# Performance work log

Measured on AMD Instinct MI355X. Metric: run time of the kernel, lower is better.

## Reference

```python
import jax, jax.numpy as jnp
import numpy as np
import math

EMBED = 1024
FF = 4096
HEADS = 16
HEAD = EMBED // HEADS
EPS = 1e-5


def new_gelu(x):
    c = math.sqrt(2.0 / math.pi)
    return 0.5 * x * (1.0 + jnp.tanh(c * (x + 0.044715 * x ** 3)))


def layer_norm(x, g, b):
    mu = jnp.mean(x, axis=-1, keepdims=True)
    var = jnp.var(x, axis=-1, keepdims=True)
    return (x - mu) * jax.lax.rsqrt(var + EPS) * g + b


def setup_inputs() -> dict:
    key = jax.random.key(0)
    ks = jax.random.split(key, 16)
    s = 0.02
    d = {
        'x': jax.random.normal(ks[0], (2, 2048, EMBED), jnp.float32),
        'Wq': jax.random.normal(ks[1], (EMBED, EMBED)) * s,
        'bq': jnp.zeros((EMBED,)),
        'Wk': jax.random.normal(ks[2], (EMBED, EMBED)) * s,
        'bk': jnp.zeros((EMBED,)),
        'Wv': jax.random.normal(ks[3], (EMBED, EMBED)) * s,
        'bv': jnp.zeros((EMBED,)),
        'Wp': jax.random.normal(ks[4], (EMBED, EMBED)) * s,
        'bp': jnp.zeros((EMBED,)),
        'W1': jax.random.normal(ks[5], (EMBED, FF)) * s,
        'b1': jnp.zeros((FF,)),
        'W2': jax.random.normal(ks[6], (FF, EMBED)) * s,
        'b2': jnp.zeros((EMBED,)),
        'g1': jnp.ones((EMBED,)), 'be1': jnp.zeros((EMBED,)),
        'g2': jnp.ones((EMBED,)), 'be2': jnp.zeros((EMBED,)),
    }
    return d


def reference(x, Wq, bq, Wk, bk, Wv, bv, Wp, bp, W1, b1, W2, b2, g1, be1, g2, be2):
    B, S, D = x.shape
    h = layer_norm(x, g1, be1)
    # project and split heads: [B,S,D] -> [B,H,S,Hd]
    def heads(y):
        return y.reshape(B, S, HEADS, HEAD).transpose(0, 2, 1, 3)
    Q = heads(h @ Wq + bq)
    K = heads(h @ Wk + bk)
    V = heads(h @ Wv + bv)
    att = jnp.einsum('bhqd,bhkd->bhqk', Q, K) / math.sqrt(HEAD)
    att = jax.nn.softmax(att, axis=-1)
    out = jnp.einsum('bhqk,bhkd->bhqd', att, V)
    out = out.transpose(0, 2, 1, 3).reshape(B, S, D)
    x = x + (out @ Wp + bp)  # dropout p=0 / eval -> identity
    h2 = layer_norm(x, g2, be2)
    x = x + (new_gelu(h2 @ W1 + b1) @ W2 + b2)
    return x
```

## Files before the change

### kernel.cpp

```cpp
#include <hip/hip_runtime.h>
#include <cstdint>


typedef __attribute__((ext_vector_type(8))) short short8;
typedef __attribute__((ext_vector_type(4))) float f32x4;

#define QSCL 0.18033688011112042f

__device__ __forceinline__ float bf2f(unsigned short u) {
    union { unsigned int i; float f; } v; v.i = ((unsigned int)u) << 16; return v.f;
}
__device__ __forceinline__ unsigned short f2bf(float f) {
    union { float f; unsigned int i; } v; v.f = f;
    unsigned int u = v.i;
    u += 0x7fff + ((u >> 16) & 1);
    return (unsigned short)(u >> 16);
}
__device__ __forceinline__ float gelu_f(float x) {
    float u = 0.7978845608028654f * (x + 0.044715f * x * x * x);
    float t = 1.f - 2.f / (__expf(2.f * u) + 1.f);
    return 0.5f * x * (1.f + t);
}
__device__ __forceinline__ void async16(const unsigned short* gp, unsigned short* lp) {
    __builtin_amdgcn_global_load_lds(
        (__attribute__((address_space(1))) void*)(gp),
        (__attribute__((address_space(3))) void*)(lp),
        16, 0, 0);
}

__device__ __forceinline__ void ln_dev(
    const float* __restrict__ x, const float* __restrict__ g,
    const float* __restrict__ b, unsigned short* __restrict__ o,
    int row, float* red)
{
    const int tid = threadIdx.x;
    const float4 v = ((const float4*)(x + (size_t)row * 1024))[tid];
    float f0 = v.x, f1 = v.y, f2 = v.z, f3 = v.w;
    float sum = f0 + f1 + f2 + f3;
    float sq  = f0 * f0 + f1 * f1 + f2 * f2 + f3 * f3;
    for (int off = 1; off < 64; off <<= 1) {
        sum += __shfl_xor(sum, off);
        sq  += __shfl_xor(sq,  off);
    }
    int wv = tid >> 6, ln = tid & 63;
    if (ln == 0) { red[wv] = sum; red[4 + wv] = sq; }
    __syncthreads();
    sum = red[0] + red[1] + red[2] + red[3];
    sq  = red[4] + red[5] + red[6] + red[7];
    float mu  = sum * (1.0f / 1024.0f);
    float var = sq  * (1.0f / 1024.0f) - mu * mu;
    float rsd = rsqrtf(fmaxf(var, 0.f) + 1e-5f);
    const float4 gg = ((const float4*)g)[tid];
    const float4 bb = ((const float4*)b)[tid];
    unsigned short* orow = o + (size_t)row * 1024;
    orow[4 * tid + 0] = f2bf((f0 - mu) * rsd * gg.x + bb.x);
    orow[4 * tid + 1] = f2bf((f1 - mu) * rsd * gg.y + bb.y);
    orow[4 * tid + 2] = f2bf((f2 - mu) * rsd * gg.z + bb.z);
    orow[4 * tid + 3] = f2bf((f3 - mu) * rsd * gg.w + bb.w);
}

__device__ __forceinline__ void transpose_dev(
    const float* __restrict__ in, unsigned short* __restrict__ out,
    int R, int C, int inStride, int bx, int by, unsigned short* tile ,
    float scale)
{
    const int tx = threadIdx.x & 15, ty = threadIdx.x >> 4;
    const int c0 = bx * 64, r0 = by * 64;
#pragma unroll
    for (int i = 0; i < 4; ++i) {
        int r = ty + 16 * i;
        float4 v = *(const float4*)(in + (size_t)(r0 + r) * inStride + c0 + tx * 4);
        tile[r * 70 + tx * 4 + 0] = f2bf(v.x * scale);
        tile[r * 70 + tx * 4 + 1] = f2bf(v.y * scale);
        tile[r * 70 + tx * 4 + 2] = f2bf(v.z * scale);
        tile[r * 70 + tx * 4 + 3] = f2bf(v.w * scale);
    }
    __syncthreads();
#pragma unroll
    for (int i = 0; i < 4; ++i) {
        int c = ty * 4 + i;
        ushort4 o;
        o.x = tile[(tx * 4 + 0) * 70 + c];
        o.y = tile[(tx * 4 + 1) * 70 + c];
        o.z = tile[(tx * 4 + 2) * 70 + c];
        o.w = tile[(tx * 4 + 3) * 70 + c];
        *(ushort4*)(out + (size_t)(c0 + c) * R + r0 + tx * 4) = o;
    }
}

__global__ __launch_bounds__(256) void ln_k(
    const float* __restrict__ x, const float* __restrict__ g,
    const float* __restrict__ b, unsigned short* __restrict__ o)
{
    __shared__ float red[8];
    ln_dev(x, g, b, o, blockIdx.x, red);
}
__global__ __launch_bounds__(256) void transpose_f2b(
    const float* __restrict__ in, unsigned short* __restrict__ out,
    int R, int C, int inStride, float scale)
{
    __shared__ unsigned short tile[64 * 70];
    transpose_dev(in, out, R, C, inStride, blockIdx.x, blockIdx.y, tile, scale);
}

__global__ __launch_bounds__(256) void prep1_k(
    const float* __restrict__ x,
    const float* __restrict__ g1, const float* __restrict__ be1,
    const float* __restrict__ Wq, const float* __restrict__ Wk,
    const float* __restrict__ Wv,
    const float* __restrict__ bq, const float* __restrict__ bk,
    const float* __restrict__ bv,
    unsigned short* __restrict__ hb,
    unsigned short* __restrict__ WTqkv,
    float* __restrict__ bcat)
{
    __shared__ unsigned short smem[64 * 70];
    const int b = blockIdx.x;
    if (b < 4096) {
        ln_dev(x, g1, be1, hb, b, (float*)smem);
    } else if (b < 4096 + 768) {
        int t = b - 4096;
        int w = t >> 8;
        int tt = t & 255;
        const float* W = (w == 0) ? Wq : (w == 1) ? Wk : Wv;
        transpose_dev(W, WTqkv + (size_t)w * 1024 * 1024,
                      1024, 1024, 1024, tt & 15, tt >> 4, smem,
                      (w == 0) ? QSCL : 1.f);
    } else {
        int i = (b - 4096 - 768) * 256 + threadIdx.x;
        float v = (i < 1024) ? bq[i] * QSCL : (i < 2048) ? bk[i - 1024] : bv[i - 2048];
        bcat[i] = v;
    }
}

__global__ __launch_bounds__(256) void prep2_k(
    const float* __restrict__ x1,
    const float* __restrict__ g2, const float* __restrict__ be2,
    const float* __restrict__ W1, const float* __restrict__ W2,
    unsigned short* __restrict__ h2,
    unsigned short* __restrict__ WT1,
    unsigned short* __restrict__ WT2)
{
    __shared__ unsigned short smem[64 * 70];
    const int b = blockIdx.x;
    if (b < 4096) {
        ln_dev(x1, g2, be2, h2, b, (float*)smem);
    } else if (b < 4096 + 1024) {
        int t = b - 4096;
        transpose_dev(W1, WT1, 1024, 4096, 4096, t & 63, t >> 6, smem, 1.f);
    } else {
        int t = b - 4096 - 1024;
        transpose_dev(W2, WT2, 4096, 1024, 1024, t & 15, t >> 4, smem, 1.f);
    }
}

__global__ __launch_bounds__(256) void vt_k(
    const unsigned short* __restrict__ src, int stride,
    unsigned short* __restrict__ Vt)
{
    __shared__ unsigned short tile[64][70];
    const int tx = threadIdx.x & 15, ty = threadIdx.x >> 4;
    const int t0 = blockIdx.x * 64;
    const int bh = blockIdx.y;
    const int bo = (bh >> 4) * 2048;
    const int ho = (bh & 15) * 64;
    const unsigned short* s = src + (size_t)bo * stride + ho;
#pragma unroll
    for (int i = 0; i < 4; ++i) {
        int r = ty + 16 * i;
        ushort4 v = *(const ushort4*)(s + (size_t)(t0 + r) * stride + tx * 4);
        tile[r][tx * 4 + 0] = v.x;
        tile[r][tx * 4 + 1] = v.y;
        tile[r][tx * 4 + 2] = v.z;
        tile[r][tx * 4 + 3] = v.w;
    }
    __syncthreads();
    unsigned short* dst = Vt + (size_t)bh * 64 * 2048;
    const int hh = tx >> 3;
    const int uu = (tx & 7) * 2;
#pragma unroll
    for (int i = 0; i < 4; ++i) {
        int d = ty * 4 + i;
        ushort4 o;
        o.x = tile[32 * hh + uu][d];
        o.y = tile[32 * hh + 16 + uu][d];
        o.z = tile[32 * hh + uu + 1][d];
        o.w = tile[32 * hh + 17 + uu][d];
        *(ushort4*)(dst + (size_t)d * 2048 + t0 + tx * 4) = o;
    }
}

__global__ __launch_bounds__(256, 3) void gemm_bt(
    const unsigned short* __restrict__ A,
    const unsigned short* __restrict__ Bt,
    const float* __restrict__ bias,
    const float* __restrict__ res,
    void* __restrict__ C,
    int M, int N, int K, int ldb, int dogelu, int out32, float bscale)
{
    __shared__ unsigned short sA[2 * 128 * 32];
    __shared__ unsigned short sB[2 * 128 * 32];
    const int tid  = threadIdx.x;
    const int wave = tid >> 6;
    const int lane = tid & 63;
    const int quad = lane >> 4;
    const int l15  = lane & 15;
    const int bm = blockIdx.y * 128;
    const int bn = blockIdx.x * 128;
    const int wM = (wave >> 1) * 64;
    const int wN = (wave & 1) * 64;

    f32x4 acc[4][4];
#pragma unroll
    for (int i = 0; i < 4; ++i)
#pragma unroll
        for (int j = 0; j < 4; ++j)
            acc[i][j] = (f32x4){0.f, 0.f, 0.f, 0.f};

    const int rowS = tid >> 2;
    const int kcS  = (tid & 3) * 8;
    const unsigned short* gA  = A  + (size_t)(bm + rowS) * K + kcS;
    const unsigned short* gA2 = gA + (size_t)64 * K;
    const unsigned short* gB  = Bt + (size_t)(bn + rowS) * ldb + kcS;
    const unsigned short* gB2 = gB + (size_t)64 * ldb;
    unsigned short* lA  = sA + tid * 8;
    unsigned short* lA2 = lA + 64 * 32;
    unsigned short* lB  = sB + tid * 8;
    unsigned short* lB2 = lB + 64 * 32;

    for (int k0 = 0; k0 < K; k0 += 64) {
        __syncthreads();
        async16(gA + k0,       lA);
        async16(gA2 + k0,      lA2);
        async16(gA + k0 + 32,  lA + 4096);
        async16(gA2 + k0 + 32, lA2 + 4096);
        async16(gB + k0,       lB);
        async16(gB2 + k0,      lB2);
        async16(gB + k0 + 32,  lB + 4096);
        async16(gB2 + k0 + 32, lB2 + 4096);
        __syncthreads();

#pragma unroll
        for (int p = 0; p < 2; ++p) {
            short8 aF[4], bF[4];
#pragma unroll
            for (int mi = 0; mi < 4; ++mi)
                aF[mi] = *(const short8*)(sA + p * 4096 + (wM + mi * 16 + l15) * 32 + quad * 8);
#pragma unroll
            for (int ni = 0; ni < 4; ++ni)
                bF[ni] = *(const short8*)(sB + p * 4096 + (wN + ni * 16 + l15) * 32 + quad * 8);
#pragma unroll
            for (int mi = 0; mi < 4; ++mi)
#pragma unroll
                for (int ni = 0; ni < 4; ++ni)
                    acc[mi][ni] = __builtin_amdgcn_mfma_f32_16x16x32_bf16(
                        aF[mi], bF[ni], acc[mi][ni], 0, 0, 0);
        }
    }

#pragma unroll
    for (int ni = 0; ni < 4; ++ni) {
        int col = bn + wN + ni * 16 + l15;
        float bv = bias ? bias[col] * bscale : 0.f;
#pragma unroll
        for (int mi = 0; mi < 4; ++mi) {
            int row = bm + wM + mi * 16 + quad * 4;
#pragma unroll
            for (int r = 0; r < 4; ++r) {
                float v = acc[mi][ni][r] + bv;
                if (dogelu) v = gelu_f(v);
                size_t idx = (size_t)(row + r) * N + col;
                if (res) v += res[idx];
                if (out32) ((float*)C)[idx] = v;
                else       ((unsigned short*)C)[idx] = f2bf(v);
            }
        }
    }
}

__global__ __launch_bounds__(256, 2) void gemm_bt64(
    const unsigned short* __restrict__ A,
    const unsigned short* __restrict__ Bt,
    const float* __restrict__ bias,
    const float* __restrict__ res,
    void* __restrict__ C,
    int M, int N, int K, int ldb, int dogelu, int out32)
{
    __shared__ unsigned short sA[4 * 128 * 32];
    __shared__ unsigned short sB[4 * 64 * 32];
    const int tid  = threadIdx.x;
    const int wave = tid >> 6;
    const int lane = tid & 63;
    const int quad = lane >> 4;
    const int l15  = lane & 15;
    const int bm = blockIdx.y * 128;
    const int bn = blockIdx.x * 64;
    const int wM = wave * 32;

    f32x4 acc[2][4];
#pragma unroll
    for (int i = 0; i < 2; ++i)
#pragma unroll
        for (int j = 0; j < 4; ++j)
            acc[i][j] = (f32x4){0.f, 0.f, 0.f, 0.f};

    const int rowS = tid >> 2;
    const int kcS  = (tid & 3) * 8;
    const unsigned short* gA  = A  + (size_t)(bm + rowS) * K + kcS;
    const unsigned short* gA2 = gA + (size_t)64 * K;
    const unsigned short* gB  = Bt + (size_t)(bn + rowS) * ldb + kcS;
    unsigned short* lA  = sA + tid * 8;
    unsigned short* lA2 = lA + 64 * 32;
    unsigned short* lB  = sB + tid * 8;

    for (int k0 = 0; k0 < K; k0 += 128) {
        __syncthreads();
#pragma unroll
        for (int p = 0; p < 4; ++p) {
            async16(gA  + k0 + p * 32, lA  + p * 4096);
            async16(gA2 + k0 + p * 32, lA2 + p * 4096);
            async16(gB  + k0 + p * 32, lB  + p * 2048);
        }
        __syncthreads();

#pragma unroll
        for (int p = 0; p < 4; ++p) {
            short8 aF[2], bF[4];
#pragma unroll
            for (int mi = 0; mi < 2; ++mi)
                aF[mi] = *(const short8*)(sA + p * 4096 + (wM + mi * 16 + l15) * 32 + quad * 8);
#pragma unroll
            for (int ni = 0; ni < 4; ++ni)
                bF[ni] = *(const short8*)(sB + p * 2048 + (ni * 16 + l15) * 32 + quad * 8);
#pragma unroll
            for (int mi = 0; mi < 2; ++mi)
#pragma unroll
                for (int ni = 0; ni < 4; ++ni)
                    acc[mi][ni] = __builtin_amdgcn_mfma_f32_16x16x32_bf16(
                        aF[mi], bF[ni], acc[mi][ni], 0, 0, 0);
        }
    }

#pragma unroll
    for (int ni = 0; ni < 4; ++ni) {
        int col = bn + ni * 16 + l15;
        float bv = bias ? bias[col] : 0.f;
#pragma unroll
        for (int mi = 0; mi < 2; ++mi) {
            int row = bm + wM + mi * 16 + quad * 4;
#pragma unroll
            for (int r = 0; r < 4; ++r) {
                float v = acc[mi][ni][r] + bv;
                if (dogelu) v = gelu_f(v);
                size_t idx = (size_t)(row + r) * N + col;
                if (res) v += res[idx];
                if (out32) ((float*)C)[idx] = v;
                else       ((unsigned short*)C)[idx] = f2bf(v);
            }
        }
    }
}

__global__ __launch_bounds__(512, 2) void attn_k(
    const unsigned short* __restrict__ Q,
    const unsigned short* __restrict__ K,
    const unsigned short* __restrict__ Vt,
    unsigned short* __restrict__ O, int qs)
{
    __shared__ unsigned short smem[45056];
    unsigned short* sK = smem;
    unsigned short* sV = smem + 2 * 5632;
    unsigned short* sP = smem + 4 * 5632;

    const int tid  = threadIdx.x;
    const int wave = tid >> 6;
    const int g    = wave & 3;
    const int h    = wave >> 2;
    const int lane = tid & 63;
    const int quad = lane >> 4;
    const int l15  = lane & 15;
    const int qb = blockIdx.x * 256;
    const int bh = blockIdx.y;
    const int bo = (bh >> 4) * 2048;
    const int ho = (bh & 15) * 64;

    const unsigned short* Qb  = Q  + (size_t)bo * qs + ho;
    const unsigned short* Kb  = K  + (size_t)bo * qs + ho;
    const unsigned short* Vtb = Vt + (size_t)bh * 64 * 2048;
    unsigned short* sPg = sP + g * 5632;
    const int ni0 = 2 * h;

    short8 qF[2][4];
#pragma unroll
    for (int ks = 0; ks < 2; ++ks)
#pragma unroll
        for (int mi = 0; mi < 4; ++mi)
            qF[ks][mi] = *(const short8*)(Qb +
                (size_t)(qb + g * 64 + mi * 16 + l15) * qs + ks * 32 + quad * 8);

    short8 onesF;
#pragma unroll
    for (int j = 0; j < 8; ++j) onesF[j] = (short)0x3F80;

    f32x4 accO[4][4];
    f32x4 accL[4];
#pragma unroll
    for (int mi = 0; mi < 4; ++mi) {
        accL[mi] = (f32x4){0.f, 0.f, 0.f, 0.f};
#pragma unroll
        for (int nd = 0; nd < 4; ++nd) accO[mi][nd] = (f32x4){0.f, 0.f, 0.f, 0.f};
    }

    const int rowS = tid >> 3;
    const int dcS  = (tid & 7) * 8;

    short8 kr, vr;
    kr = *(const short8*)(Kb + (size_t)rowS * qs + dcS);
    vr = *(const short8*)(Vtb + (size_t)rowS * 2048 + dcS);
    *(short8*)(sK + rowS * 88 + dcS) = kr;
    *(short8*)(sV + rowS * 88 + dcS) = vr;
    kr = *(const short8*)(Kb + (size_t)(64 + rowS) * qs + dcS);
    vr = *(const short8*)(Vtb + (size_t)rowS * 2048 + 64 + dcS);

    for (int kt = 0; kt < 2048; kt += 64) {
        const int buf = (kt >> 6) & 1;
        __syncthreads();

        short8 bK[2][2];
#pragma unroll
        for (int ks = 0; ks < 2; ++ks)
#pragma unroll
            for (int nj = 0; nj < 2; ++nj)
                bK[ks][nj] = *(const short8*)(sK + buf * 5632 +
                    ((ni0 + nj) * 16 + l15) * 88 + ks * 32 + quad * 8);

        f32x4 s0[4], s1[4];
#pragma unroll
        for (int mi = 0; mi < 4; ++mi) {
            s0[mi] = (f32x4){0.f, 0.f, 0.f, 0.f};
            s1[mi] = s0[mi];
#pragma unroll
            for (int ks = 0; ks < 2; ++ks) {
                s0[mi] = __builtin_amdgcn_mfma_f32_16x16x32_bf16(qF[ks][mi], bK[ks][0], s0[mi], 0, 0, 0);
                s1[mi] = __builtin_amdgcn_mfma_f32_16x16x32_bf16(qF[ks][mi], bK[ks][1], s1[mi], 0, 0, 0);
            }
        }

        if (kt + 64 < 2048) {
            *(short8*)(sK + (buf ^ 1) * 5632 + rowS * 88 + dcS) = kr;
            *(short8*)(sV + (buf ^ 1) * 5632 + rowS * 88 + dcS) = vr;
            if (kt + 128 < 2048) {
                kr = *(const short8*)(Kb + (size_t)(kt + 128 + rowS) * qs + dcS);
                vr = *(const short8*)(Vtb + (size_t)rowS * 2048 + kt + 128 + dcS);
            }
        }

#pragma unroll
        for (int mi = 0; mi < 4; ++mi)
#pragma unroll
            for (int r = 0; r < 4; ++r) {
                float p0 = __builtin_amdgcn_exp2f(s0[mi][r]);
                float p1 = __builtin_amdgcn_exp2f(s1[mi][r]);
                unsigned int w;
                asm("v_cvt_pk_bf16_f32 %0, %1, %2" : "=v"(w) : "v"(p0), "v"(p1));
                *(unsigned int*)(sPg + (mi * 16 + quad * 4 + r) * 88 + h * 32 + l15 * 2) = w;
            }

        short8 aP[4], bV[4];
#pragma unroll
        for (int nd = 0; nd < 4; ++nd)
            bV[nd] = *(const short8*)(sV + buf * 5632 + (nd * 16 + l15) * 88 + h * 32 + quad * 8);
#pragma unroll
        for (int mi = 0; mi < 4; ++mi)
            aP[mi] = *(const short8*)(sPg + (mi * 16 + l15) * 88 + h * 32 + quad * 8);

        __builtin_amdgcn_s_setprio(1);
#pragma unroll
        for (int mi = 0; mi < 4; ++mi) {
#pragma unroll
            for (int nd = 0; nd < 4; ++nd)
                accO[mi][nd] = __builtin_amdgcn_mfma_f32_16x16x32_bf16(
                    aP[mi], bV[nd], accO[mi][nd], 0, 0, 0);
            accL[mi] = __builtin_amdgcn_mfma_f32_16x16x32_bf16(
                aP[mi], onesF, accL[mi], 0, 0, 0);
        }
        __builtin_amdgcn_s_setprio(0);
    }

    __syncthreads();
    float* scr = (float*)smem;
    float* po = scr + (size_t)(g * 64 + lane) * 68;
    float* pl = scr + 17408 + (size_t)(g * 64 + lane) * 20;
    if (h == 1) {
#pragma unroll
        for (int mi = 0; mi < 4; ++mi) {
#pragma unroll
            for (int nd = 0; nd < 4; ++nd)
                *(f32x4*)(po + mi * 16 + nd * 4) = accO[mi][nd];
            *(f32x4*)(pl + mi * 4) = accL[mi];
        }
    }
    __syncthreads();
    if (h == 0) {
#pragma unroll
        for (int mi = 0; mi < 4; ++mi) {
            accL[mi] += *(const f32x4*)(pl + mi * 4);
#pragma unroll
            for (int nd = 0; nd < 4; ++nd)
                accO[mi][nd] += *(const f32x4*)(po + mi * 16 + nd * 4);
        }
#pragma unroll
        for (int mi = 0; mi < 4; ++mi)
#pragma unroll
            for (int r = 0; r < 4; ++r) {
                int row = qb + g * 64 + mi * 16 + quad * 4 + r;
                float inv = 1.f / accL[mi][r];
#pragma unroll
                for (int nd = 0; nd < 4; ++nd)
                    O[(size_t)(bo + row) * 1024 + ho + nd * 16 + l15] =
                        f2bf(accO[mi][nd][r] * inv);
            }
    }
}

extern "C" void kernel_launch(void* const* d_in, const int* in_sizes, int n_in,
                              void* d_out, int out_size, void* d_ws, size_t ws_size,
                              hipStream_t stream)
{
    (void)in_sizes; (void)n_in; (void)out_size;
    const float* x   = (const float*)d_in[0];
    const float* Wq  = (const float*)d_in[1];
    const float* bq  = (const float*)d_in[2];
    const float* Wk  = (const float*)d_in[3];
    const float* bk  = (const float*)d_in[4];
    const float* Wv  = (const float*)d_in[5];
    const float* bv  = (const float*)d_in[6];
    const float* Wp  = (const float*)d_in[7];
    const float* bp  = (const float*)d_in[8];
    const float* W1  = (const float*)d_in[9];
    const float* b1  = (const float*)d_in[10];
    const float* W2  = (const float*)d_in[11];
    const float* b2  = (const float*)d_in[12];
    const float* g1  = (const float*)d_in[13];
    const float* be1 = (const float*)d_in[14];
    const float* g2  = (const float*)d_in[15];
    const float* be2 = (const float*)d_in[16];
    float* out = (float*)d_out;

    char* ws = (char*)d_ws;
    char* dob = (char*)d_out;
    const size_t MB = 1024 * 1024;

    if (ws_size >= 40 * MB) {
        unsigned short* hb    = (unsigned short*)dob;
        unsigned short* WTqkv = (unsigned short*)(dob + 8 * MB);
        float*          bcat  = (float*)(dob + 14 * MB);
        unsigned short* QKV   = (unsigned short*)ws;
        unsigned short* att   = (unsigned short*)(ws + 24 * MB);
        unsigned short* Vt    = (unsigned short*)(ws + 32 * MB);
        unsigned short* WTp   = (unsigned short*)(ws + 32 * MB);
        unsigned short* h2    = (unsigned short*)ws;
        unsigned short* WT1   = (unsigned short*)(ws + 8 * MB);
        unsigned short* WT2   = (unsigned short*)(ws + 16 * MB);
        unsigned short* act   = (unsigned short*)(ws + 24 * MB);

        prep1_k<<<4096 + 768 + 12, 256, 0, stream>>>(
            x, g1, be1, Wq, Wk, Wv, bq, bk, bv, hb, WTqkv, bcat);
        gemm_bt<<<dim3(24, 32), 256, 0, stream>>>(hb, WTqkv, bcat, nullptr, QKV,
                                                  4096, 3072, 1024, 1024, 0, 0, 1.f);
        vt_k<<<dim3(32, 32), 256, 0, stream>>>(QKV + 2048, 3072, Vt);
        attn_k<<<dim3(8, 32), 512, 0, stream>>>(QKV, QKV + 1024, Vt, att, 3072);
        transpose_f2b<<<dim3(16, 16), 256, 0, stream>>>(Wp, WTp, 1024, 1024, 1024, 1.f);
        gemm_bt64<<<dim3(16, 32), 256, 0, stream>>>(att, WTp, bp, x, out,
                                                    4096, 1024, 1024, 1024, 0, 1);
        prep2_k<<<4096 + 2048, 256, 0, stream>>>(out, g2, be2, W1, W2, h2, WT1, WT2);
        for (int c = 0; c < 2; ++c) {
            gemm_bt<<<dim3(16, 32), 256, 0, stream>>>(h2, WT1 + (size_t)c * 2048 * 1024,
                                                      b1 + c * 2048, nullptr, act,
                                                      4096, 2048, 1024, 1024, 1, 0, 1.f);
            gemm_bt64<<<dim3(16, 32), 256, 0, stream>>>(act, WT2 + (size_t)c * 2048,
                                                        c == 0 ? b2 : nullptr, out, out,
                                                        4096, 1024, 2048, 4096, 0, 1);
        }
    } else {
        unsigned short* Qw  = (unsigned short*)(ws);
        unsigned short* Kw  = (unsigned short*)(ws + 8 * MB);
        unsigned short* Vw  = (unsigned short*)(ws + 16 * MB);
        unsigned short* hb  = (unsigned short*)dob;
        unsigned short* WTq = (unsigned short*)(dob + 8 * MB);
        unsigned short* VtF = (unsigned short*)(dob + 8 * MB);
        unsigned short* att = Qw;
        unsigned short* WTb = Kw;
        unsigned short* h2  = Vw;
        unsigned short* act = Qw;

        ln_k<<<4096, 256, 0, stream>>>(x, g1, be1, hb);
        transpose_f2b<<<dim3(16, 16), 256, 0, stream>>>(Wq, WTq, 1024, 1024, 1024, QSCL);
        gemm_bt<<<dim3(8, 32), 256, 0, stream>>>(hb, WTq, bq, nullptr, Qw, 4096, 1024, 1024, 1024, 0, 0, QSCL);
        transpose_f2b<<<dim3(16, 16), 256, 0, stream>>>(Wk, WTq, 1024, 1024, 1024, 1.f);
        gemm_bt<<<dim3(8, 32), 256, 0, stream>>>(hb, WTq, bk, nullptr, Kw, 4096, 1024, 1024, 1024, 0, 0, 1.f);
        transpose_f2b<<<dim3(16, 16), 256, 0, stream>>>(Wv, WTq, 1024, 1024, 1024, 1.f);
        gemm_bt<<<dim3(8, 32), 256, 0, stream>>>(hb, WTq, bv, nullptr, Vw, 4096, 1024, 1024, 1024, 0, 0, 1.f);
        vt_k<<<dim3(32, 32), 256, 0, stream>>>(Vw, 1024, VtF);
        attn_k<<<dim3(8, 32), 512, 0, stream>>>(Qw, Kw, VtF, att, 1024);
        transpose_f2b<<<dim3(16, 16), 256, 0, stream>>>(Wp, WTb, 1024, 1024, 1024, 1.f);
        gemm_bt64<<<dim3(16, 32), 256, 0, stream>>>(att, WTb, bp, x, out, 4096, 1024, 1024, 1024, 0, 1);
        ln_k<<<4096, 256, 0, stream>>>(out, g2, be2, h2);
        for (int c = 0; c < 4; ++c) {
            transpose_f2b<<<dim3(16, 16), 256, 0, stream>>>(W1 + c * 1024, WTb, 1024, 1024, 4096, 1.f);
            gemm_bt64<<<dim3(16, 32), 256, 0, stream>>>(h2, WTb, b1 + c * 1024, nullptr, act,
                                                        4096, 1024, 1024, 1024, 1, 0);
            unsigned short* WT2c = WTb + 1024 * 1024;
            transpose_f2b<<<dim3(16, 16), 256, 0, stream>>>(W2 + (size_t)c * 1024 * 1024, WT2c,
                                                            1024, 1024, 1024, 1.f);
            gemm_bt64<<<dim3(16, 32), 256, 0, stream>>>(act, WT2c, c == 0 ? b2 : nullptr,
                                                        out, out, 4096, 1024, 1024, 1024, 0, 1);
        }
    }
}
```

Measured before the change: 379.6 us.

## Process two key tiles per barrier in attention and remap blocks

The attention kernel now stages two 64-key K/V tiles per iteration, using four LDS buffers. This halves the number of block-wide barriers and prefetches 128 keys ahead. Block indices are remapped so that neighbouring blocks cover different heads and query tiles, and launch bounds drop to one block per SM, which shared memory usage already forced. The GEMM K-step is cut from 128 to 64, halving its LDS footprint at the cost of twice as many barrier pairs per K loop.

```diff
diff --git a/kernel.cpp b/kernel.cpp
--- a/kernel.cpp
+++ b/kernel.cpp
@@ -286,8 +286,8 @@
     void* __restrict__ C,
     int M, int N, int K, int ldb, int dogelu, int out32)
 {
-    __shared__ unsigned short sA[4 * 128 * 32];
-    __shared__ unsigned short sB[4 * 64 * 32];
+    __shared__ unsigned short sA[2 * 128 * 32];
+    __shared__ unsigned short sB[2 * 64 * 32];
     const int tid  = threadIdx.x;
     const int wave = tid >> 6;
     const int lane = tid & 63;
@@ -313,18 +313,18 @@
     unsigned short* lA2 = lA + 64 * 32;
     unsigned short* lB  = sB + tid * 8;
 
-    for (int k0 = 0; k0 < K; k0 += 128) {
+    for (int k0 = 0; k0 < K; k0 += 64) {
         __syncthreads();
-#pragma unroll
-        for (int p = 0; p < 4; ++p) {
-            async16(gA  + k0 + p * 32, lA  + p * 4096);
-            async16(gA2 + k0 + p * 32, lA2 + p * 4096);
-            async16(gB  + k0 + p * 32, lB  + p * 2048);
-        }
+        async16(gA + k0,       lA);
+        async16(gA2 + k0,      lA2);
+        async16(gA + k0 + 32,  lA + 4096);
+        async16(gA2 + k0 + 32, lA2 + 4096);
+        async16(gB + k0,       lB);
+        async16(gB + k0 + 32,  lB + 2048);
         __syncthreads();
 
 #pragma unroll
-        for (int p = 0; p < 4; ++p) {
+        for (int p = 0; p < 2; ++p) {
             short8 aF[2], bF[4];
 #pragma unroll
             for (int mi = 0; mi < 2; ++mi)
@@ -361,16 +361,16 @@
     }
 }
 
-__global__ __launch_bounds__(512, 2) void attn_k(
+__global__ __launch_bounds__(512, 1) void attn_k(
     const unsigned short* __restrict__ Q,
     const unsigned short* __restrict__ K,
     const unsigned short* __restrict__ Vt,
     unsigned short* __restrict__ O, int qs)
 {
-    __shared__ unsigned short smem[45056];
+    __shared__ unsigned short smem[67584];
     unsigned short* sK = smem;
-    unsigned short* sV = smem + 2 * 5632;
-    unsigned short* sP = smem + 4 * 5632;
+    unsigned short* sV = smem + 4 * 5632;
+    unsigned short* sP = smem + 8 * 5632;
 
     const int tid  = threadIdx.x;
     const int wave = tid >> 6;
@@ -379,8 +379,8 @@
     const int lane = tid & 63;
     const int quad = lane >> 4;
     const int l15  = lane & 15;
-    const int qb = blockIdx.x * 256;
-    const int bh = blockIdx.y;
+    const int bh = blockIdx.x * 4 + (blockIdx.y & 3);
+    const int qb = (blockIdx.y >> 2) * 256;
     const int bo = (bh >> 4) * 2048;
     const int ho = (bh & 15) * 64;
 
@@ -414,77 +414,98 @@
     const int rowS = tid >> 3;
     const int dcS  = (tid & 7) * 8;
 
-    short8 kr, vr;
-    kr = *(const short8*)(Kb + (size_t)rowS * qs + dcS);
-    vr = *(const short8*)(Vtb + (size_t)rowS * 2048 + dcS);
-    *(short8*)(sK + rowS * 88 + dcS) = kr;
-    *(short8*)(sV + rowS * 88 + dcS) = vr;
-    kr = *(const short8*)(Kb + (size_t)(64 + rowS) * qs + dcS);
-    vr = *(const short8*)(Vtb + (size_t)rowS * 2048 + 64 + dcS);
-
-    for (int kt = 0; kt < 2048; kt += 64) {
-        const int buf = (kt >> 6) & 1;
+    short8 kr[2], vr[2];
+#pragma unroll
+    for (int s = 0; s < 2; ++s) {
+        kr[s] = *(const short8*)(Kb + (size_t)(s * 64 + rowS) * qs + dcS);
+        vr[s] = *(const short8*)(Vtb + (size_t)rowS * 2048 + s * 64 + dcS);
+    }
+#pragma unroll
+    for (int s = 0; s < 2; ++s) {
+        *(short8*)(sK + s * 5632 + rowS * 88 + dcS) = kr[s];
+        *(short8*)(sV + s * 5632 + rowS * 88 + dcS) = vr[s];
+    }
+#pragma unroll
+    for (int s = 0; s < 2; ++s) {
+        kr[s] = *(const short8*)(Kb + (size_t)(128 + s * 64 + rowS) * qs + dcS);
+        vr[s] = *(const short8*)(Vtb + (size_t)rowS * 2048 + 128 + s * 64 + dcS);
+    }
+
+    for (int kt = 0; kt < 2048; kt += 128) {
+        const int buf = (kt >> 7) & 1;
         __syncthreads();
 
-        short8 bK[2][2];
-#pragma unroll
-        for (int ks = 0; ks < 2; ++ks)
-#pragma unroll
-            for (int nj = 0; nj < 2; ++nj)
-                bK[ks][nj] = *(const short8*)(sK + buf * 5632 +
-                    ((ni0 + nj) * 16 + l15) * 88 + ks * 32 + quad * 8);
-
-        f32x4 s0[4], s1[4];
-#pragma unroll
-        for (int mi = 0; mi < 4; ++mi) {
-            s0[mi] = (f32x4){0.f, 0.f, 0.f, 0.f};
-            s1[mi] = s0[mi];
-#pragma unroll
-            for (int ks = 0; ks < 2; ++ks) {
-                s0[mi] = __builtin_amdgcn_mfma_f32_16x16x32_bf16(qF[ks][mi], bK[ks][0], s0[mi], 0, 0, 0);
-                s1[mi] = __builtin_amdgcn_mfma_f32_16x16x32_bf16(qF[ks][mi], bK[ks][1], s1[mi], 0, 0, 0);
+#pragma unroll
+        for (int s = 0; s < 2; ++s) {
+            const unsigned short* sKb = sK + (buf * 2 + s) * 5632;
+            const unsigned short* sVb = sV + (buf * 2 + s) * 5632;
+
+            short8 bK[2][2];
+#pragma unroll
+            for (int ks = 0; ks < 2; ++ks)
+#pragma unroll
+                for (int nj = 0; nj < 2; ++nj)
+                    bK[ks][nj] = *(const short8*)(sKb +
+                        ((ni0 + nj) * 16 + l15) * 88 + ks * 32 + quad * 8);
+
+            f32x4 s0[4], s1[4];
+#pragma unroll
+            for (int mi = 0; mi < 4; ++mi) {
+                s0[mi] = (f32x4){0.f, 0.f, 0.f, 0.f};
+                s1[mi] = s0[mi];
+#pragma unroll
+                for (int ks = 0; ks < 2; ++ks) {
+                    s0[mi] = __builtin_amdgcn_mfma_f32_16x16x32_bf16(qF[ks][mi], bK[ks][0], s0[mi], 0, 0, 0);
+                    s1[mi] = __builtin_amdgcn_mfma_f32_16x16x32_bf16(qF[ks][mi], bK[ks][1], s1[mi], 0, 0, 0);
+                }
             }
-        }
-
-        if (kt + 64 < 2048) {
-            *(short8*)(sK + (buf ^ 1) * 5632 + rowS * 88 + dcS) = kr;
-            *(short8*)(sV + (buf ^ 1) * 5632 + rowS * 88 + dcS) = vr;
-            if (kt + 128 < 2048) {
-                kr = *(const short8*)(Kb + (size_t)(kt + 128 + rowS) * qs + dcS);
-                vr = *(const short8*)(Vtb + (size_t)rowS * 2048 + kt + 128 + dcS);
+
+            if (s == 0 && kt + 128 < 2048) {
+#pragma unroll
+                for (int t = 0; t < 2; ++t) {
+                    *(short8*)(sK + ((buf ^ 1) * 2 + t) * 5632 + rowS * 88 + dcS) = kr[t];
+                    *(short8*)(sV + ((buf ^ 1) * 2 + t) * 5632 + rowS * 88 + dcS) = vr[t];
+                }
+                if (kt + 256 < 2048) {
+#pragma unroll
+                    for (int t = 0; t < 2; ++t) {
+                        kr[t] = *(const short8*)(Kb + (size_t)(kt + 256 + t * 64 + rowS) * qs + dcS);
+                        vr[t] = *(const short8*)(Vtb + (size_t)rowS * 2048 + kt + 256 + t * 64 + dcS);
+                    }
+                }
             }
-        }
-
-#pragma unroll
-        for (int mi = 0; mi < 4; ++mi)
-#pragma unroll
-            for (int r = 0; r < 4; ++r) {
-                float p0 = __builtin_amdgcn_exp2f(s0[mi][r]);
-                float p1 = __builtin_amdgcn_exp2f(s1[mi][r]);
-                unsigned int w;
-                asm("v_cvt_pk_bf16_f32 %0, %1, %2" : "=v"(w) : "v"(p0), "v"(p1));
-                *(unsigned int*)(sPg + (mi * 16 + quad * 4 + r) * 88 + h * 32 + l15 * 2) = w;
+
+#pragma unroll
+            for (int mi = 0; mi < 4; ++mi)
+#pragma unroll
+                for (int r = 0; r < 4; ++r) {
+                    float p0 = __builtin_amdgcn_exp2f(s0[mi][r]);
+                    float p1 = __builtin_amdgcn_exp2f(s1[mi][r]);
+                    unsigned int w;
+                    asm("v_cvt_pk_bf16_f32 %0, %1, %2" : "=v"(w) : "v"(p0), "v"(p1));
+                    *(unsigned int*)(sPg + (mi * 16 + quad * 4 + r) * 88 + h * 32 + l15 * 2) = w;
+                }
+
+            short8 aP[4], bV[4];
+#pragma unroll
+            for (int nd = 0; nd < 4; ++nd)
+                bV[nd] = *(const short8*)(sVb + (nd * 16 + l15) * 88 + h * 32 + quad * 8);
+#pragma unroll
+            for (int mi = 0; mi < 4; ++mi)
+                aP[mi] = *(const short8*)(sPg + (mi * 16 + l15) * 88 + h * 32 + quad * 8);
+
+            __builtin_amdgcn_s_setprio(1);
+#pragma unroll
+            for (int mi = 0; mi < 4; ++mi) {
+#pragma unroll
+                for (int nd = 0; nd < 4; ++nd)
+                    accO[mi][nd] = __builtin_amdgcn_mfma_f32_16x16x32_bf16(
+                        aP[mi], bV[nd], accO[mi][nd], 0, 0, 0);
+                accL[mi] = __builtin_amdgcn_mfma_f32_16x16x32_bf16(
+                    aP[mi], onesF, accL[mi], 0, 0, 0);
             }
-
-        short8 aP[4], bV[4];
-#pragma unroll
-        for (int nd = 0; nd < 4; ++nd)
-            bV[nd] = *(const short8*)(sV + buf * 5632 + (nd * 16 + l15) * 88 + h * 32 + quad * 8);
-#pragma unroll
-        for (int mi = 0; mi < 4; ++mi)
-            aP[mi] = *(const short8*)(sPg + (mi * 16 + l15) * 88 + h * 32 + quad * 8);
-
-        __builtin_amdgcn_s_setprio(1);
-#pragma unroll
-        for (int mi = 0; mi < 4; ++mi) {
-#pragma unroll
-            for (int nd = 0; nd < 4; ++nd)
-                accO[mi][nd] = __builtin_amdgcn_mfma_f32_16x16x32_bf16(
-                    aP[mi], bV[nd], accO[mi][nd], 0, 0, 0);
-            accL[mi] = __builtin_amdgcn_mfma_f32_16x16x32_bf16(
-                aP[mi], onesF, accL[mi], 0, 0, 0);
-        }
-        __builtin_amdgcn_s_setprio(0);
+            __builtin_amdgcn_s_setprio(0);
+        }
     }
 
     __syncthreads();
```

Result: no change. 378.4 us (-0.3%).
